# Kernel optimization log

Measured on AMD Instinct MI355X. Metric: run time of the kernel, lower is better.

Reference implementation:

```python
import jax, jax.numpy as jnp
import numpy as np

# Modulated deformable conv2d (torchvision semantics): per kernel tap, sample the
# input at a runtime-offset location via bilinear interpolation (zero padding
# outside the image), modulate with mask, then do the weighted accumulation.

STRIDE = (1, 1)
PADDING = (1, 1)
DILATION = (1, 1)


def deform_conv2d(x, offset, mask, weight, bias):
    B, C, H, W = x.shape
    O, Cg, kh, kw = weight.shape
    K = kh * kw
    og = offset.shape[1] // (2 * K)          # offset groups
    Ho, Wo = offset.shape[2], offset.shape[3]
    sh, sw = STRIDE
    ph, pw = PADDING
    dh, dw = DILATION

    off = offset.reshape(B, og, K, 2, Ho, Wo)
    ki = jnp.arange(K)
    base_ky = ((ki // kw) * dh).astype(x.dtype)            # [K]
    base_kx = ((ki % kw) * dw).astype(x.dtype)
    base_h = (jnp.arange(Ho) * sh - ph).astype(x.dtype)    # [Ho]
    base_w = (jnp.arange(Wo) * sw - pw).astype(x.dtype)    # [Wo]
    # sampling positions, [B, og, K, Ho, Wo]
    p_y = off[:, :, :, 0] + base_ky[None, None, :, None, None] + base_h[None, None, None, :, None]
    p_x = off[:, :, :, 1] + base_kx[None, None, :, None, None] + base_w[None, None, None, None, :]

    y0 = jnp.floor(p_y)
    x0 = jnp.floor(p_x)
    ly = p_y - y0
    lx = p_x - x0
    y0i = y0.astype(jnp.int32)
    x0i = x0.astype(jnp.int32)

    Cog = C // og
    x_flat = x.reshape(B, og, Cog, H * W)

    def gather(yi, xi):
        valid = ((yi >= 0) & (yi < H) & (xi >= 0) & (xi < W))
        idx = jnp.clip(yi, 0, H - 1) * W + jnp.clip(xi, 0, W - 1)
        idx_flat = idx.reshape(B, og, 1, K * Ho * Wo)
        v = jnp.take_along_axis(x_flat, idx_flat, axis=3).reshape(B, og, Cog, K, Ho, Wo)
        return v * valid[:, :, None].astype(x.dtype)

    w00 = ((1 - ly) * (1 - lx))[:, :, None]
    w01 = ((1 - ly) * lx)[:, :, None]
    w10 = (ly * (1 - lx))[:, :, None]
    w11 = (ly * lx)[:, :, None]
    val = (w00 * gather(y0i, x0i) + w01 * gather(y0i, x0i + 1)
           + w10 * gather(y0i + 1, x0i) + w11 * gather(y0i + 1, x0i + 1))

    if mask is not None:
        val = val * mask.reshape(B, og, K, Ho, Wo)[:, :, None]

    # grouped conv accumulation over sampled taps
    G = C // Cg                               # conv groups (=1 here)
    val = val.reshape(B, G, C // G, K, Ho, Wo)
    w = weight.reshape(G, O // G, Cg, K)
    out = jnp.einsum('bgckhw,gock->bgohw', val, w).reshape(B, O, Ho, Wo)
    if bias is not None:
        out = out + bias[None, :, None, None]
    return out


def setup_inputs() -> dict:
    key = jax.random.key(0)
    k1, k2, k3, k4, k5 = jax.random.split(key, 5)
    B, C, H, W = 4, 64, 128, 128
    O, kh, kw = 64, 3, 3
    return {
        'input': jax.random.normal(k1, (B, C, H, W), dtype=jnp.float32),
        'offset': jax.random.normal(k2, (B, 2 * kh * kw, H, W), dtype=jnp.float32),
        'mask': jax.random.uniform(k3, (B, kh * kw, H, W), dtype=jnp.float32),
        'weight': jax.random.normal(k4, (O, C, kh, kw), dtype=jnp.float32) * (1.0 / np.sqrt(C * kh * kw)),
        'bias': jax.random.normal(k5, (O,), dtype=jnp.float32) * 0.01,
    }


def reference(input, offset, mask, weight, bias):
    return deform_conv2d(input, offset, mask, weight, bias)
```

## Files before the change

kernel.cpp:

```cpp
#include <hip/hip_runtime.h>


#define BB 4
#define CC 64
#define HH 128
#define WW 128
#define OO 64
#define KHW 3
#define KK 9
#define HW (HH * WW)

typedef __bf16 bf16_t;
typedef bf16_t bf16x8 __attribute__((ext_vector_type(8)));
typedef float f32x4 __attribute__((ext_vector_type(4)));

__global__ __launch_bounds__(256) void prep_kernel(const float* __restrict__ x,
                                                   bf16_t* __restrict__ xt,
                                                   const float* __restrict__ w,
                                                   bf16_t* __restrict__ wf) {
    __shared__ float tile[64 * 65];
    const int t = threadIdx.x;
    if (blockIdx.x < BB * 256) {
        const int b  = blockIdx.x >> 8;
        const int p0 = (blockIdx.x & 255) << 6;
#pragma unroll
        for (int i = 0; i < 16; ++i) {
            int c = i * 4 + (t >> 6);
            int p = t & 63;
            tile[c * 65 + p] = x[(b * CC + c) * HW + p0 + p];
        }
        __syncthreads();
#pragma unroll
        for (int i = 0; i < 16; ++i) {
            int p = i * 4 + (t >> 6);
            int c = t & 63;
            xt[(size_t)((b * HW) + p0 + p) * CC + c] = (bf16_t)tile[c * 65 + p];
        }
    } else {
        int i = (blockIdx.x - BB * 256) * 256 + t;
        if (i >= OO * CC * KK) return;
        int j    = i & 7;
        int lane = (i >> 3) & 63;
        int nt   = (i >> 9) & 3;
        int q    = (i >> 11) & 1;
        int k    = i >> 12;
        int o = nt * 16 + (lane & 15);
        int c = q * 32 + ((lane >> 4) << 3) + j;
        wf[i] = (bf16_t)w[(o * CC + c) * KK + k];
    }
}

__global__ __launch_bounds__(256, 4) void deform_conv_mfma(
    const bf16_t* __restrict__ xt, const float* __restrict__ offset,
    const float* __restrict__ mask, const bf16x8* __restrict__ wf,
    const float* __restrict__ bias, float* __restrict__ out) {
    const int t    = threadIdx.x;
    const int wg   = (blockIdx.x & 7) * ((BB * 256) >> 3) + (blockIdx.x >> 3);
    const int b    = wg >> 8;
    const int p0   = (wg & 255) << 6;
    const int lane = t & 63;
    const int wv   = t >> 6;
    const int m0   = wv << 4;
    const int col  = lane & 15;
    const int quad = lane >> 4;
    const int rem  = p0 + m0 + col;
    const int ho   = rem >> 7;
    const int wo   = rem & (WW - 1);
    const int cb   = quad << 3;
    const float fho = (float)(ho - 1);
    const float fwo = (float)(wo - 1);

    const bf16_t* xb  = xt + (size_t)b * HW * CC;
    const float* offp = offset + (size_t)b * (2 * KK) * HW + rem;
    const float* mp   = mask + (size_t)b * KK * HW + rem;

    f32x4 acc[4];
#pragma unroll
    for (int nt = 0; nt < 4; ++nt) acc[nt] = (f32x4){0.f, 0.f, 0.f, 0.f};

    float syA, sxA, smA, syB, sxB, smB;
    float wA0, wA1, wA2, wA3, wB0, wB1, wB2, wB3;
    bf16x8 gA00, gA01, gA10, gA11, hA00, hA01, hA10, hA11;
    bf16x8 gB00, gB01, gB10, gB11, hB00, hB01, hB10, hB11;
    bf16x8 af0, af1;

#define LOADS(k_, P_)                                                         \
    if ((k_) < KK) {                                                          \
        sy##P_ = offp[(2 * (k_)) * HW];                                       \
        sx##P_ = offp[(2 * (k_) + 1) * HW];                                   \
        sm##P_ = mp[(k_) * HW];                                               \
    }

#define ISSUE(k_, P_)                                                         \
    {                                                                         \
        float py = sy##P_ + (float)((k_) / KHW) + fho;                        \
        float px = sx##P_ + (float)((k_) % KHW) + fwo;                        \
        float fy0 = floorf(py), fx0 = floorf(px);                             \
        float ly = py - fy0, lx = px - fx0;                                   \
        int y0 = (int)fy0, x0 = (int)fx0;                                     \
        int y1 = y0 + 1, x1 = x0 + 1;                                         \
        bool vy0 = (y0 >= 0) && (y0 < HH), vy1 = (y1 >= 0) && (y1 < HH);      \
        bool vx0 = (x0 >= 0) && (x0 < WW), vx1 = (x1 >= 0) && (x1 < WW);      \
        int cy0 = min(max(y0, 0), HH - 1), cy1 = min(max(y1, 0), HH - 1);     \
        int cx0 = min(max(x0, 0), WW - 1), cx1 = min(max(x1, 0), WW - 1);     \
        float mmv = sm##P_;                                                   \
        w##P_##0 = (vy0 && vx0) ? mmv * (1.0f - ly) * (1.0f - lx) : 0.0f;     \
        w##P_##1 = (vy0 && vx1) ? mmv * (1.0f - ly) * lx : 0.0f;              \
        w##P_##2 = (vy1 && vx0) ? mmv * ly * (1.0f - lx) : 0.0f;              \
        w##P_##3 = (vy1 && vx1) ? mmv * ly * lx : 0.0f;                       \
        const bf16_t* b00 = xb + (size_t)(cy0 * WW + cx0) * CC + cb;          \
        const bf16_t* b01 = xb + (size_t)(cy0 * WW + cx1) * CC + cb;          \
        const bf16_t* b10 = xb + (size_t)(cy1 * WW + cx0) * CC + cb;          \
        const bf16_t* b11 = xb + (size_t)(cy1 * WW + cx1) * CC + cb;          \
        g##P_##00 = *(const bf16x8*)b00; h##P_##00 = *(const bf16x8*)(b00 + 32); \
        g##P_##01 = *(const bf16x8*)b01; h##P_##01 = *(const bf16x8*)(b01 + 32); \
        g##P_##10 = *(const bf16x8*)b10; h##P_##10 = *(const bf16x8*)(b10 + 32); \
        g##P_##11 = *(const bf16x8*)b11; h##P_##11 = *(const bf16x8*)(b11 + 32); \
    }

#define BLEND(P_)                                                             \
    {                                                                         \
        _Pragma("unroll") for (int i = 0; i < 8; ++i) {                       \
            float v = w##P_##0 * (float)g##P_##00[i] +                        \
                      w##P_##1 * (float)g##P_##01[i] +                        \
                      w##P_##2 * (float)g##P_##10[i] +                        \
                      w##P_##3 * (float)g##P_##11[i];                         \
            af0[i] = (bf16_t)v;                                               \
        }                                                                     \
        _Pragma("unroll") for (int i = 0; i < 8; ++i) {                       \
            float v = w##P_##0 * (float)h##P_##00[i] +                        \
                      w##P_##1 * (float)h##P_##01[i] +                        \
                      w##P_##2 * (float)h##P_##10[i] +                        \
                      w##P_##3 * (float)h##P_##11[i];                         \
            af1[i] = (bf16_t)v;                                               \
        }                                                                     \
    }

#define MFMAS(k_)                                                             \
    {                                                                         \
        _Pragma("unroll") for (int nt = 0; nt < 4; ++nt) {                    \
            bf16x8 bfg = wf[((k_) * 8 + nt) * 64 + lane];                     \
            acc[nt] = __builtin_amdgcn_mfma_f32_16x16x32_bf16(                \
                af0, bfg, acc[nt], 0, 0, 0);                                  \
        }                                                                     \
        _Pragma("unroll") for (int nt = 0; nt < 4; ++nt) {                    \
            bf16x8 bfg = wf[((k_) * 8 + 4 + nt) * 64 + lane];                 \
            acc[nt] = __builtin_amdgcn_mfma_f32_16x16x32_bf16(                \
                af1, bfg, acc[nt], 0, 0, 0);                                  \
        }                                                                     \
    }

#define BODY(k_, P_, Q_)                                                      \
    {                                                                         \
        if ((k_) + 1 < KK) ISSUE((k_) + 1, Q_);                               \
        LOADS((k_) + 2, P_);                                                  \
        BLEND(P_);                                                            \
        MFMAS(k_);                                                            \
    }

    LOADS(0, A)
    LOADS(1, B)
    ISSUE(0, A);

    BODY(0, A, B)
    BODY(1, B, A)
    BODY(2, A, B)
    BODY(3, B, A)
    BODY(4, A, B)
    BODY(5, B, A)
    BODY(6, A, B)
    BODY(7, B, A)
    BODY(8, A, B)

#undef BODY
#undef MFMAS
#undef BLEND
#undef ISSUE
#undef LOADS

#pragma unroll
    for (int nt = 0; nt < 4; ++nt) {
        int o = nt * 16 + col;
        float bv = bias[o];
        f32x4 r = acc[nt];
        r.x += bv; r.y += bv; r.z += bv; r.w += bv;
        float* dst = out + (size_t)(b * OO + o) * HW + p0 + m0 + quad * 4;
        *(f32x4*)dst = r;
    }
}

extern "C" void kernel_launch(void* const* d_in, const int* in_sizes, int n_in,
                              void* d_out, int out_size, void* d_ws,
                              size_t ws_size, hipStream_t stream) {
    const float* x      = (const float*)d_in[0];
    const float* offset = (const float*)d_in[1];
    const float* mask   = (const float*)d_in[2];
    const float* weight = (const float*)d_in[3];
    const float* bias   = (const float*)d_in[4];
    float* out = (float*)d_out;

    bf16_t* xt  = (bf16_t*)d_ws;
    bf16_t* wfr = (bf16_t*)((char*)d_ws + (size_t)BB * HW * CC * 2);

    int nwf_blocks = (OO * CC * KK + 255) / 256;
    prep_kernel<<<BB * 256 + nwf_blocks, 256, 0, stream>>>(x, xt, weight, wfr);

    deform_conv_mfma<<<BB * (HW / 64), 256, 0, stream>>>(
        xt, offset, mask, (const bf16x8*)wfr, bias, out);
}
```

Before: 121.5 us.

## Stage 2D input halo tile in shared memory for deformable bilinear gathers

Each block now covers an 8x8 spatial output tile instead of a 64-pixel row strip. It preloads a 16x16 pixel halo window (all 64 channels, bf16) into XOR-swizzled LDS and serves bilinear corner reads from it, falling back to global loads only when a corner with nonzero weight lies outside the window. The prep transpose also switches to vectorized 16-byte stores, and a scheduling barrier separates gather issue from blend. The trade is 32KB of LDS per block, which lowers occupancy, plus extra sync and branch divergence on the fallback path.

```diff
diff --git a/kernel.cpp b/kernel.cpp
--- a/kernel.cpp
+++ b/kernel.cpp
@@ -30,12 +30,17 @@
             tile[c * 65 + p] = x[(b * CC + c) * HW + p0 + p];
         }
         __syncthreads();
-#pragma unroll
-        for (int i = 0; i < 16; ++i) {
-            int p = i * 4 + (t >> 6);
-            int c = t & 63;
-            xt[(size_t)((b * HW) + p0 + p) * CC + c] = (bf16_t)tile[c * 65 + p];
-        }
+        const int p = t >> 2;
+        const int q = t & 3;
+        bf16x8 v0, v1;
+#pragma unroll
+        for (int e = 0; e < 8; ++e) v0[e] = (bf16_t)tile[(q * 8 + e) * 65 + p];
+#pragma unroll
+        for (int e = 0; e < 8; ++e)
+            v1[e] = (bf16_t)tile[((q + 4) * 8 + e) * 65 + p];
+        bf16_t* dst = xt + (size_t)((b * HW) + p0 + p) * CC;
+        *(bf16x8*)(dst + q * 8) = v0;
+        *(bf16x8*)(dst + (q + 4) * 8) = v1;
     } else {
         int i = (blockIdx.x - BB * 256) * 256 + t;
         if (i >= OO * CC * KK) return;
@@ -57,22 +62,39 @@
     const int t    = threadIdx.x;
     const int wg   = (blockIdx.x & 7) * ((BB * 256) >> 3) + (blockIdx.x >> 3);
     const int b    = wg >> 8;
-    const int p0   = (wg & 255) << 6;
+    const int ti   = wg & 255;
+    const int r0   = ((ti >> 4) << 3);
+    const int c0   = ((ti & 15) << 3);
     const int lane = t & 63;
     const int wv   = t >> 6;
-    const int m0   = wv << 4;
     const int col  = lane & 15;
     const int quad = lane >> 4;
-    const int rem  = p0 + m0 + col;
-    const int ho   = rem >> 7;
-    const int wo   = rem & (WW - 1);
+    const int prow = r0 + 2 * wv + (col >> 3);
+    const int pcol = c0 + (col & 7);
+    const int rem  = prow * WW + pcol;
+    const int wy0  = r0 - 4;
+    const int wx0  = c0 - 4;
     const int cb   = quad << 3;
-    const float fho = (float)(ho - 1);
-    const float fwo = (float)(wo - 1);
+
+    __shared__ bf16_t V[256 * 64];
 
     const bf16_t* xb  = xt + (size_t)b * HW * CC;
     const float* offp = offset + (size_t)b * (2 * KK) * HW + rem;
     const float* mp   = mask + (size_t)b * KK * HW + rem;
+
+    {
+        const int i  = t >> 4;
+        const int j  = t & 15;
+        const int cy = min(max(wy0 + i, 0), HH - 1);
+        const int cx = min(max(wx0 + j, 0), WW - 1);
+        const bf16_t* src = xb + (size_t)(cy * WW + cx) * CC;
+        bf16_t* dst = &V[(i * 16 + j) * 64];
+        const int sw = (j & 7) * 8;
+#pragma unroll
+        for (int s = 0; s < 8; ++s)
+            *(bf16x8*)(dst + ((s * 8) ^ sw)) = *(const bf16x8*)(src + s * 8);
+    }
+    __syncthreads();
 
     f32x4 acc[4];
 #pragma unroll
@@ -93,8 +115,8 @@
 
 #define ISSUE(k_, P_)                                                         \
     {                                                                         \
-        float py = sy##P_ + (float)((k_) / KHW) + fho;                        \
-        float px = sx##P_ + (float)((k_) % KHW) + fwo;                        \
+        float py = sy##P_ + (float)((k_) / KHW) + (float)(prow - 1);          \
+        float px = sx##P_ + (float)((k_) % KHW) + (float)(pcol - 1);          \
         float fy0 = floorf(py), fx0 = floorf(px);                             \
         float ly = py - fy0, lx = px - fx0;                                   \
         int y0 = (int)fy0, x0 = (int)fx0;                                     \
@@ -108,14 +130,43 @@
         w##P_##1 = (vy0 && vx1) ? mmv * (1.0f - ly) * lx : 0.0f;              \
         w##P_##2 = (vy1 && vx0) ? mmv * ly * (1.0f - lx) : 0.0f;              \
         w##P_##3 = (vy1 && vx1) ? mmv * ly * lx : 0.0f;                       \
-        const bf16_t* b00 = xb + (size_t)(cy0 * WW + cx0) * CC + cb;          \
-        const bf16_t* b01 = xb + (size_t)(cy0 * WW + cx1) * CC + cb;          \
-        const bf16_t* b10 = xb + (size_t)(cy1 * WW + cx0) * CC + cb;          \
-        const bf16_t* b11 = xb + (size_t)(cy1 * WW + cx1) * CC + cb;          \
-        g##P_##00 = *(const bf16x8*)b00; h##P_##00 = *(const bf16x8*)(b00 + 32); \
-        g##P_##01 = *(const bf16x8*)b01; h##P_##01 = *(const bf16x8*)(b01 + 32); \
-        g##P_##10 = *(const bf16x8*)b10; h##P_##10 = *(const bf16x8*)(b10 + 32); \
-        g##P_##11 = *(const bf16x8*)b11; h##P_##11 = *(const bf16x8*)(b11 + 32); \
+        int uy0 = y0 - wy0, ux0 = x0 - wx0;                                   \
+        int uy1 = uy0 + 1, ux1 = ux0 + 1;                                     \
+        bool iy0 = (unsigned)uy0 < 16u, iy1 = (unsigned)uy1 < 16u;            \
+        bool ix0 = (unsigned)ux0 < 16u, ix1 = (unsigned)ux1 < 16u;            \
+        int qy0 = min(max(uy0, 0), 15), qy1 = min(max(uy1, 0), 15);           \
+        int qx0 = min(max(ux0, 0), 15), qx1 = min(max(ux1, 0), 15);           \
+        int pa = (qy0 * 16 + qx0) * 64, pb = (qy0 * 16 + qx1) * 64;           \
+        int pc = (qy1 * 16 + qx0) * 64, pd = (qy1 * 16 + qx1) * 64;           \
+        int sa = (qx0 & 7), sb = (qx1 & 7);                                   \
+        g##P_##00 = *(const bf16x8*)&V[pa + ((quad ^ sa) << 3)];              \
+        h##P_##00 = *(const bf16x8*)&V[pa + (((4 + quad) ^ sa) << 3)];        \
+        g##P_##01 = *(const bf16x8*)&V[pb + ((quad ^ sb) << 3)];              \
+        h##P_##01 = *(const bf16x8*)&V[pb + (((4 + quad) ^ sb) << 3)];        \
+        g##P_##10 = *(const bf16x8*)&V[pc + ((quad ^ sa) << 3)];              \
+        h##P_##10 = *(const bf16x8*)&V[pc + (((4 + quad) ^ sa) << 3)];        \
+        g##P_##11 = *(const bf16x8*)&V[pd + ((quad ^ sb) << 3)];              \
+        h##P_##11 = *(const bf16x8*)&V[pd + (((4 + quad) ^ sb) << 3)];        \
+        if (w##P_##0 != 0.0f && !(iy0 && ix0)) {                              \
+            const bf16_t* p = xb + (size_t)(cy0 * WW + cx0) * CC + cb;        \
+            g##P_##00 = *(const bf16x8*)p;                                    \
+            h##P_##00 = *(const bf16x8*)(p + 32);                             \
+        }                                                                     \
+        if (w##P_##1 != 0.0f && !(iy0 && ix1)) {                              \
+            const bf16_t* p = xb + (size_t)(cy0 * WW + cx1) * CC + cb;        \
+            g##P_##01 = *(const bf16x8*)p;                                    \
+            h##P_##01 = *(const bf16x8*)(p + 32);                             \
+        }                                                                     \
+        if (w##P_##2 != 0.0f && !(iy1 && ix0)) {                              \
+            const bf16_t* p = xb + (size_t)(cy1 * WW + cx0) * CC + cb;        \
+            g##P_##10 = *(const bf16x8*)p;                                    \
+            h##P_##10 = *(const bf16x8*)(p + 32);                             \
+        }                                                                     \
+        if (w##P_##3 != 0.0f && !(iy1 && ix1)) {                              \
+            const bf16_t* p = xb + (size_t)(cy1 * WW + cx1) * CC + cb;        \
+            g##P_##11 = *(const bf16x8*)p;                                    \
+            h##P_##11 = *(const bf16x8*)(p + 32);                             \
+        }                                                                     \
     }
 
 #define BLEND(P_)                                                             \
@@ -154,6 +205,7 @@
     {                                                                         \
         if ((k_) + 1 < KK) ISSUE((k_) + 1, Q_);                               \
         LOADS((k_) + 2, P_);                                                  \
+        __builtin_amdgcn_sched_barrier(0);                                    \
         BLEND(P_);                                                            \
         MFMAS(k_);                                                            \
     }
@@ -184,7 +236,8 @@
         float bv = bias[o];
         f32x4 r = acc[nt];
         r.x += bv; r.y += bv; r.z += bv; r.w += bv;
-        float* dst = out + (size_t)(b * OO + o) * HW + p0 + m0 + quad * 4;
+        float* dst = out + (size_t)(b * OO + o) * HW +
+                     (r0 + 2 * wv + (quad >> 1)) * WW + c0 + (quad & 1) * 4;
         *(f32x4*)dst = r;
     }
 }
```

Measured after the change: 103.6 us. 1.17x faster.
